# Optimization experiments

Hardware: AMD Instinct MI355X
Metric: run time of the kernel (lower is better)

## Reference

```python
import jax, jax.numpy as jnp
import numpy as np
import math

D_MODEL = 1024
N_HEADS = 16
D_K = D_MODEL // N_HEADS
B, S = 4, 2048


def setup_inputs() -> dict:
    key = jax.random.key(0)
    ks = jax.random.split(key, 11)
    std = 1.0 / math.sqrt(D_MODEL)
    inp = {
        "query": jax.random.normal(ks[0], (B, S, D_MODEL), dtype=jnp.float32),
        "key_in": jax.random.normal(ks[1], (B, S, D_MODEL), dtype=jnp.float32),
        "value": jax.random.normal(ks[2], (B, S, D_MODEL), dtype=jnp.float32),
        "Wq": jax.random.normal(ks[3], (D_MODEL, D_MODEL), dtype=jnp.float32) * std,
        "bq": jnp.zeros((D_MODEL,), dtype=jnp.float32),
        "Wk": jax.random.normal(ks[4], (D_MODEL, D_MODEL), dtype=jnp.float32) * std,
        "bk": jnp.zeros((D_MODEL,), dtype=jnp.float32),
        "Wv": jax.random.normal(ks[5], (D_MODEL, D_MODEL), dtype=jnp.float32) * std,
        "bv": jnp.zeros((D_MODEL,), dtype=jnp.float32),
        "Wo": jax.random.normal(ks[6], (D_MODEL, D_MODEL), dtype=jnp.float32) * std,
        "bo": jnp.zeros((D_MODEL,), dtype=jnp.float32),
    }
    return inp


def reference(query, key_in, value, Wq, bq, Wk, bk, Wv, bv, Wo, bo):
    b, s, _ = query.shape
    scale = math.sqrt(D_K)
    # projections: nn.Linear computes x @ W.T + b
    Q = (query @ Wq.T + bq).reshape(b, s, N_HEADS, D_K).transpose(0, 2, 1, 3)
    K = (key_in @ Wk.T + bk).reshape(b, s, N_HEADS, D_K).transpose(0, 2, 1, 3)
    V = (value @ Wv.T + bv).reshape(b, s, N_HEADS, D_K).transpose(0, 2, 1, 3)
    # [b, h, s, s]
    scores = jnp.einsum("bhqd,bhkd->bhqk", Q, K) / scale
    causal = jnp.tril(jnp.ones((s, s), dtype=bool))
    scores = jnp.where(causal[None, None, :, :], scores, jnp.float32(-1e9))
    attn = jax.nn.softmax(scores, axis=-1)
    out = jnp.einsum("bhqk,bhkd->bhqd", attn, V)
    out = out.transpose(0, 2, 1, 3).reshape(b, s, D_MODEL)
    return out @ Wo.T + bo
```

## Files before the change

kernel.cpp:

```cpp
#include <hip/hip_runtime.h>
#include <hip/hip_bf16.h>
#include <cstdint>

#define DM   1024
#define NH   16
#define DKK  64
#define BB   4
#define SS   2048

typedef __attribute__((ext_vector_type(8)))  short short8;
typedef __attribute__((ext_vector_type(4)))  float f32x4;
typedef __attribute__((ext_vector_type(16))) float f32x16;

__device__ __forceinline__ unsigned short f2bf(float f) {
    union { float f; uint32_t u; } v; v.f = f;
    uint32_t u = v.u;
    uint32_t r = (u + 0x7FFFu + ((u >> 16) & 1u)) >> 16;
    return (unsigned short)r;
}

#define GLL(src, dst) __builtin_amdgcn_global_load_lds(                      \
        (__attribute__((address_space(1))) void*)(src),                      \
        (__attribute__((address_space(3))) void*)(dst), 16, 0, 0)

__global__ void cvt_w(const float* __restrict__ wq, const float* __restrict__ wk,
                      const float* __restrict__ wv, const float* __restrict__ wo,
                      unsigned short* __restrict__ dst)
{
    int i = blockIdx.x * 256 + threadIdx.x;
    int a = i >> 17;
    int r = i & 131071;
    int j = r >> 7, kb = r & 127;
    int kbs = (kb & ~7) | ((kb ^ j) & 7);
    const float* s = (a == 0 ? wq : a == 1 ? wk : a == 2 ? wv : wo) + (size_t)j * 1024 + kbs * 8;
    float4 f0 = *(const float4*)(s);
    float4 f1 = *(const float4*)(s + 4);
    union { uint32_t u[4]; short8 s8; } c;
    asm("v_cvt_pk_bf16_f32 %0, %1, %2" : "=v"(c.u[0]) : "v"(f0.x), "v"(f0.y));
    asm("v_cvt_pk_bf16_f32 %0, %1, %2" : "=v"(c.u[1]) : "v"(f0.z), "v"(f0.w));
    asm("v_cvt_pk_bf16_f32 %0, %1, %2" : "=v"(c.u[2]) : "v"(f1.x), "v"(f1.y));
    asm("v_cvt_pk_bf16_f32 %0, %1, %2" : "=v"(c.u[3]) : "v"(f1.z), "v"(f1.w));
    *(short8*)(dst + ((size_t)a << 20) + (size_t)j * 1024 + kb * 8) = c.s8;
}

__global__ __launch_bounds__(256) void gemm_qkv(
        const float* __restrict__ Aq, const float* __restrict__ Ak, const float* __restrict__ Av,
        const unsigned short* __restrict__ Wq, const unsigned short* __restrict__ Wk,
        const unsigned short* __restrict__ Wv,
        const float* __restrict__ bq, const float* __restrict__ bk, const float* __restrict__ bv,
        unsigned short* __restrict__ Qo, unsigned short* __restrict__ Ko,
        unsigned short* __restrict__ Vo, const float qscale)
{
    const int orig = blockIdx.z * 512 + blockIdx.y * 8 + blockIdx.x;
    const int wid  = (orig & 7) * 192 + (orig >> 3);
    const int z    = wid >> 9;
    const int rem  = wid & 511;
    const int brow = (rem >> 3) * 128;
    const int bcol = (rem & 7) * 128;

    const float* A           = (z == 0) ? Aq : (z == 1) ? Ak : Av;
    const unsigned short* Bw = (z == 0) ? Wq : (z == 1) ? Wk : Wv;
    const float* bias        = (z == 0) ? bq : (z == 1) ? bk : bv;

    __shared__ __align__(16) unsigned short lA[128 * 64];
    __shared__ __align__(16) unsigned short lB[2][128 * 64];

    const int tid = threadIdx.x;
    const int w = tid >> 6, l = tid & 63;
    const int wr = (w >> 1) * 64, wc = (w & 1) * 64;
    const int lrow = l & 15;
    const int hi = l >> 4;
    const int sr = l >> 3, scb = l & 7;

    const float* aga[4];
    const unsigned short* bga[4];
    int awb[4], lbo[4];
#pragma unroll
    for (int i = 0; i < 4; ++i) {
        const int chunk = w * 4 + i;
        const int r = chunk * 8 + sr;
        aga[i] = A + (size_t)(brow + r) * 1024 + scb * 8;
        bga[i] = Bw + (size_t)(bcol + r) * 1024 + scb * 8;
        awb[i] = chunk * 1024 + sr * 128 + ((scb ^ sr) << 4);
        lbo[i] = chunk * 512;
    }

    f32x4 aX[4][2], aY[4][2];
    f32x4 acc[4][4] = {};

#pragma unroll
    for (int i = 0; i < 4; ++i) GLL(bga[i], lB[0] + lbo[i]);
#pragma unroll
    for (int i = 0; i < 4; ++i) { aX[i][0] = *(const f32x4*)(aga[i]); aX[i][1] = *(const f32x4*)(aga[i] + 4); }
#pragma unroll
    for (int i = 0; i < 4; ++i) { aY[i][0] = *(const f32x4*)(aga[i] + 64); aY[i][1] = *(const f32x4*)(aga[i] + 64 + 4); }

#define QKV_CVT(CUR)                                                                              \
    _Pragma("unroll")                                                                             \
    for (int i = 0; i < 4; ++i) {                                                                 \
        union { uint32_t u[4]; short8 s8; } c;                                                    \
        asm("v_cvt_pk_bf16_f32 %0, %1, %2" : "=v"(c.u[0]) : "v"(CUR[i][0][0]), "v"(CUR[i][0][1]));\
        asm("v_cvt_pk_bf16_f32 %0, %1, %2" : "=v"(c.u[1]) : "v"(CUR[i][0][2]), "v"(CUR[i][0][3]));\
        asm("v_cvt_pk_bf16_f32 %0, %1, %2" : "=v"(c.u[2]) : "v"(CUR[i][1][0]), "v"(CUR[i][1][1]));\
        asm("v_cvt_pk_bf16_f32 %0, %1, %2" : "=v"(c.u[3]) : "v"(CUR[i][1][2]), "v"(CUR[i][1][3]));\
        *(short8*)((char*)lA + awb[i]) = c.s8;                                                    \
    }

#define QKV_MFMA(LB)                                                                              \
    {                                                                                             \
        const unsigned short* lb = (LB);                                                          \
        __builtin_amdgcn_s_setprio(1);                                                            \
        _Pragma("unroll")                                                                         \
        for (int kk = 0; kk < 2; ++kk) {                                                          \
            short8 af[4], bf[4];                                                                  \
            _Pragma("unroll")                                                                     \
            for (int m = 0; m < 4; ++m) {                                                         \
                const int row = wr + m * 16 + lrow;                                               \
                const int pb = (kk * 4 + hi) ^ (row & 7);                                         \
                af[m] = *(const short8*)((const char*)lA + row * 128 + (pb << 4));                \
            }                                                                                     \
            _Pragma("unroll")                                                                     \
            for (int n = 0; n < 4; ++n) {                                                         \
                const int row = wc + n * 16 + lrow;                                               \
                const int pb = (kk * 4 + hi) ^ (row & 7);                                         \
                bf[n] = *(const short8*)((const char*)lb + row * 128 + (pb << 4));                \
            }                                                                                     \
            _Pragma("unroll")                                                                     \
            for (int m = 0; m < 4; ++m)                                                           \
                _Pragma("unroll")                                                                 \
                for (int n = 0; n < 4; ++n)                                                       \
                    acc[m][n] = __builtin_amdgcn_mfma_f32_16x16x32_bf16(af[m], bf[n], acc[m][n], 0, 0, 0); \
        }                                                                                         \
        __builtin_amdgcn_s_setprio(0);                                                            \
    }

    for (int t = 0; t < 14; t += 2) {
        QKV_CVT(aX);
        {
            const int ko = (t + 2) * 64;
#pragma unroll
            for (int i = 0; i < 4; ++i) { aX[i][0] = *(const f32x4*)(aga[i] + ko); aX[i][1] = *(const f32x4*)(aga[i] + ko + 4); }
            const int kb = (t + 1) * 64;
#pragma unroll
            for (int i = 0; i < 4; ++i) GLL(bga[i] + kb, lB[1] + lbo[i]);
        }
        asm volatile("s_waitcnt vmcnt(12) lgkmcnt(0)" ::: "memory");
        __builtin_amdgcn_s_barrier();
        QKV_MFMA(lB[0]);
        asm volatile("" ::: "memory");
        __builtin_amdgcn_s_barrier();
        QKV_CVT(aY);
        {
            const int ko = (t + 3) * 64;
#pragma unroll
            for (int i = 0; i < 4; ++i) { aY[i][0] = *(const f32x4*)(aga[i] + ko); aY[i][1] = *(const f32x4*)(aga[i] + ko + 4); }
            const int kb = (t + 2) * 64;
#pragma unroll
            for (int i = 0; i < 4; ++i) GLL(bga[i] + kb, lB[0] + lbo[i]);
        }
        asm volatile("s_waitcnt vmcnt(12) lgkmcnt(0)" ::: "memory");
        __builtin_amdgcn_s_barrier();
        QKV_MFMA(lB[1]);
        asm volatile("" ::: "memory");
        __builtin_amdgcn_s_barrier();
    }
    QKV_CVT(aX);
#pragma unroll
    for (int i = 0; i < 4; ++i) GLL(bga[i] + 15 * 64, lB[1] + lbo[i]);
    asm volatile("s_waitcnt vmcnt(4) lgkmcnt(0)" ::: "memory");
    __builtin_amdgcn_s_barrier();
    QKV_MFMA(lB[0]);
    asm volatile("" ::: "memory");
    __builtin_amdgcn_s_barrier();
    QKV_CVT(aY);
    asm volatile("s_waitcnt vmcnt(0) lgkmcnt(0)" ::: "memory");
    __builtin_amdgcn_s_barrier();
    QKV_MFMA(lB[1]);

    const float ascale = (z == 0) ? qscale : 1.0f;
#pragma unroll
    for (int m = 0; m < 4; ++m) {
#pragma unroll
        for (int n = 0; n < 4; ++n) {
            const int i0 = brow + wr + m * 16 + (l >> 4) * 4;
            const int j  = bcol + wc + n * 16 + lrow;
            const float bj = bias[j];
            const int hh = j >> 6, d = j & 63;
            if (z < 2) {
                unsigned short* Cb = (z == 0) ? Qo : Ko;
#pragma unroll
                for (int t = 0; t < 4; ++t) {
                    const int i = i0 + t;
                    const int b = i >> 11, s = i & 2047;
                    Cb[(((size_t)(b * NH + hh) * SS) + s) * DKK + d] = f2bf((acc[m][n][t] + bj) * ascale);
                }
            } else {
                const int b = i0 >> 11, s0 = i0 & 2047;
                ushort4 pk;
                pk.x = f2bf(acc[m][n][0] + bj);
                pk.y = f2bf(acc[m][n][1] + bj);
                pk.z = f2bf(acc[m][n][2] + bj);
                pk.w = f2bf(acc[m][n][3] + bj);
                *(ushort4*)(Vo + (((size_t)(b * NH + hh) * DKK) + d) * SS + s0) = pk;
            }
        }
    }
#undef QKV_CVT
#undef QKV_MFMA
}

__global__ __launch_bounds__(256) void gemm_out(
        const unsigned short* __restrict__ A,
        const unsigned short* __restrict__ Bw,
        const float* __restrict__ bias,
        float* __restrict__ Cout)
{
    const int orig = blockIdx.y * 8 + blockIdx.x;
    const int wid  = (orig & 7) * 64 + (orig >> 3);
    const int brow = (wid >> 3) * 128;
    const int bcol = (wid & 7) * 128;

    __shared__ __align__(16) unsigned short lA[128 * 64];
    __shared__ __align__(16) unsigned short lB[2][128 * 64];

    const int tid = threadIdx.x;
    const int w = tid >> 6, l = tid & 63;
    const int wr = (w >> 1) * 64, wc = (w & 1) * 64;
    const int lrow = l & 15;
    const int hi = l >> 4;
    const int sr = l >> 3, scb = l & 7;

    const unsigned short* aga[4];
    const unsigned short* bga[4];
    int awb[4], lbo[4];
#pragma unroll
    for (int i = 0; i < 4; ++i) {
        const int chunk = w * 4 + i;
        const int r = chunk * 8 + sr;
        aga[i] = A  + (size_t)(brow + r) * 1024 + scb * 8;
        bga[i] = Bw + (size_t)(bcol + r) * 1024 + scb * 8;
        awb[i] = chunk * 1024 + sr * 128 + ((scb ^ sr) << 4);
        lbo[i] = chunk * 512;
    }

    short8 aX[4], aY[4];
    f32x4 acc[4][4] = {};

#pragma unroll
    for (int i = 0; i < 4; ++i) GLL(bga[i], lB[0] + lbo[i]);
#pragma unroll
    for (int i = 0; i < 4; ++i) aX[i] = *(const short8*)(aga[i]);
#pragma unroll
    for (int i = 0; i < 4; ++i) aY[i] = *(const short8*)(aga[i] + 64);

#define OUT_WR(CUR)                                                     \
    _Pragma("unroll")                                                   \
    for (int i = 0; i < 4; ++i)                                         \
        *(short8*)((char*)lA + awb[i]) = CUR[i];

#define OUT_MFMA(LB)                                                                              \
    {                                                                                             \
        const unsigned short* lb = (LB);                                                          \
        __builtin_amdgcn_s_setprio(1);                                                            \
        _Pragma("unroll")                                                                         \
        for (int kk = 0; kk < 2; ++kk) {                                                          \
            short8 af[4], bf[4];                                                                  \
            _Pragma("unroll")                                                                     \
            for (int m = 0; m < 4; ++m) {                                                         \
                const int row = wr + m * 16 + lrow;                                               \
                const int pb = (kk * 4 + hi) ^ (row & 7);                                         \
                af[m] = *(const short8*)((const char*)lA + row * 128 + (pb << 4));                \
            }                                                                                     \
            _Pragma("unroll")                                                                     \
            for (int n = 0; n < 4; ++n) {                                                         \
                const int row = wc + n * 16 + lrow;                                               \
                const int pb = (kk * 4 + hi) ^ (row & 7);                                         \
                bf[n] = *(const short8*)((const char*)lb + row * 128 + (pb << 4));                \
            }                                                                                     \
            _Pragma("unroll")                                                                     \
            for (int m = 0; m < 4; ++m)                                                           \
                _Pragma("unroll")                                                                 \
                for (int n = 0; n < 4; ++n)                                                       \
                    acc[m][n] = __builtin_amdgcn_mfma_f32_16x16x32_bf16(af[m], bf[n], acc[m][n], 0, 0, 0); \
        }                                                                                         \
        __builtin_amdgcn_s_setprio(0);                                                            \
    }

    for (int t = 0; t < 14; t += 2) {
        OUT_WR(aX);
        {
            const int ko = (t + 2) * 64;
#pragma unroll
            for (int i = 0; i < 4; ++i) aX[i] = *(const short8*)(aga[i] + ko);
            const int kb = (t + 1) * 64;
#pragma unroll
            for (int i = 0; i < 4; ++i) GLL(bga[i] + kb, lB[1] + lbo[i]);
        }
        asm volatile("s_waitcnt vmcnt(8) lgkmcnt(0)" ::: "memory");
        __builtin_amdgcn_s_barrier();
        OUT_MFMA(lB[0]);
        asm volatile("" ::: "memory");
        __builtin_amdgcn_s_barrier();

        OUT_WR(aY);
        {
            const int ko = (t + 3) * 64;
#pragma unroll
            for (int i = 0; i < 4; ++i) aY[i] = *(const short8*)(aga[i] + ko);
            const int kb = (t + 2) * 64;
#pragma unroll
            for (int i = 0; i < 4; ++i) GLL(bga[i] + kb, lB[0] + lbo[i]);
        }
        asm volatile("s_waitcnt vmcnt(8) lgkmcnt(0)" ::: "memory");
        __builtin_amdgcn_s_barrier();
        OUT_MFMA(lB[1]);
        asm volatile("" ::: "memory");
        __builtin_amdgcn_s_barrier();
    }
    OUT_WR(aX);
#pragma unroll
    for (int i = 0; i < 4; ++i) GLL(bga[i] + 15 * 64, lB[1] + lbo[i]);
    asm volatile("s_waitcnt vmcnt(4) lgkmcnt(0)" ::: "memory");
    __builtin_amdgcn_s_barrier();
    OUT_MFMA(lB[0]);
    asm volatile("" ::: "memory");
    __builtin_amdgcn_s_barrier();
    OUT_WR(aY);
    asm volatile("s_waitcnt vmcnt(0) lgkmcnt(0)" ::: "memory");
    __builtin_amdgcn_s_barrier();
    OUT_MFMA(lB[1]);

#pragma unroll
    for (int m = 0; m < 4; ++m) {
#pragma unroll
        for (int n = 0; n < 4; ++n) {
            const int i0 = brow + wr + m * 16 + (l >> 4) * 4;
            const int j  = bcol + wc + n * 16 + lrow;
            const float bj = bias[j];
#pragma unroll
            for (int t = 0; t < 4; ++t)
                Cout[(size_t)(i0 + t) * DM + j] = acc[m][n][t] + bj;
        }
    }
#undef OUT_WR
#undef OUT_MFMA
}

__global__ __launch_bounds__(256) void attn_kernel(
        const unsigned short* __restrict__ Q,
        const unsigned short* __restrict__ K,
        const unsigned short* __restrict__ Vt,
        unsigned short* __restrict__ AO)
{
    const int flat = blockIdx.y * 16 + blockIdx.x;
    const int r8 = flat & 7, k8 = flat >> 3;
    const int bh = r8 * 8 + (k8 & 7);
    const int qchunk = 15 - (k8 >> 3);
    const int tid = threadIdx.x;
    const int w = tid >> 6, l = tid & 63;
    const int ln = l & 31, h = l >> 5;
    const int qb = qchunk * 128;
    const int q0w = qb + w * 32;

    __shared__ __align__(16) char lK[2][4096];
    __shared__ __align__(16) char lV[2][4096];

    const unsigned short* Qp = Q  + ((size_t)bh * SS + q0w) * DKK;
    const unsigned short* Kp = K  + (size_t)bh * SS * DKK;
    const unsigned short* Vp = Vt + (size_t)bh * DKK * SS;

    const int srow = tid >> 3, scb = tid & 7;
    const int swb = srow * 128 + ((scb * 16) ^ ((srow & 7) << 4));
    const unsigned short* ksrc = Kp + srow * DKK + scb * 8;
    const int vd = (scb < 4) ? srow : (srow + 32);
    const unsigned short* vsrc = Vp + (size_t)vd * SS + (scb & 3) * 8;

    int ka[4], va[4];
#pragma unroll
    for (int ks = 0; ks < 4; ++ks)
        ka[ks] = ln * 128 + ((ks * 32 + h * 16) ^ ((ln & 7) << 4));
#pragma unroll
    for (int c = 0; c < 4; ++c)
        va[c] = ln * 128 + ((c * 32 + h * 16) ^ ((ln & 7) << 4));

    short8 qf[4];
#pragma unroll
    for (int ks = 0; ks < 4; ++ks)
        qf[ks] = *(const short8*)(Qp + (size_t)ln * DKK + ks * 16 + h * 8);

    f32x16 o0 = {}, o1 = {};
    float lsum = 0.f;

    const int Tc = qb / 32;
    const int NT = Tc + 4;

    auto compute = [&](int t, int buf) {
        const char* kb = lK[buf];
        const char* vb = lV[buf];
        short8 kf[4];
#pragma unroll
        for (int ks = 0; ks < 4; ++ks) kf[ks] = *(const short8*)(kb + ka[ks]);

        f32x16 s = {};
        __builtin_amdgcn_s_setprio(1);
#pragma unroll
        for (int ks = 0; ks < 4; ++ks)
            s = __builtin_amdgcn_mfma_f32_32x32x16_bf16(kf[ks], qf[ks], s, 0, 0, 0);
        __builtin_amdgcn_s_setprio(0);

        const bool diag = (t == Tc + w);
#pragma unroll
        for (int r = 0; r < 16; ++r) {
            float e;
            asm("v_exp_f32 %0, %1" : "=v"(e) : "v"(s[r]));
            if (diag) {
                const int crow = (r & 3) + 8 * (r >> 2) + 4 * h;
                e = (crow > ln) ? 0.f : e;
            }
            s[r] = e;
            lsum += e;
        }

        uint32_t pk[8];
#pragma unroll
        for (int i = 0; i < 8; ++i) {
            uint32_t d;
            asm("v_cvt_pk_bf16_f32 %0, %1, %2" : "=v"(d) : "v"(s[2 * i]), "v"(s[2 * i + 1]));
            pk[i] = d;
        }
        asm("v_permlane32_swap_b32 %0, %1" : "+v"(pk[0]), "+v"(pk[2]));
        asm("v_permlane32_swap_b32 %0, %1" : "+v"(pk[1]), "+v"(pk[3]));
        asm("v_permlane32_swap_b32 %0, %1" : "+v"(pk[4]), "+v"(pk[6]));
        asm("v_permlane32_swap_b32 %0, %1" : "+v"(pk[5]), "+v"(pk[7]));

        union Ux { uint32_t u[4]; short8 s8; } pa0, pa1;
        pa0.u[0] = pk[0]; pa0.u[1] = pk[1]; pa0.u[2] = pk[2]; pa0.u[3] = pk[3];
        pa1.u[0] = pk[4]; pa1.u[1] = pk[5]; pa1.u[2] = pk[6]; pa1.u[3] = pk[7];

        short8 vf00 = *(const short8*)(vb + va[0]);
        short8 vf10 = *(const short8*)(vb + va[1]);
        short8 vf01 = *(const short8*)(vb + va[2]);
        short8 vf11 = *(const short8*)(vb + va[3]);

        __builtin_amdgcn_s_setprio(1);
        o0 = __builtin_amdgcn_mfma_f32_32x32x16_bf16(pa0.s8, vf00, o0, 0, 0, 0);
        o0 = __builtin_amdgcn_mfma_f32_32x32x16_bf16(pa1.s8, vf10, o0, 0, 0, 0);
        o1 = __builtin_amdgcn_mfma_f32_32x32x16_bf16(pa0.s8, vf01, o1, 0, 0, 0);
        o1 = __builtin_amdgcn_mfma_f32_32x32x16_bf16(pa1.s8, vf11, o1, 0, 0, 0);
        __builtin_amdgcn_s_setprio(0);
    };

    short8 kA = *(const short8*)(ksrc);
    short8 vA = *(const short8*)(vsrc);
    *(short8*)(&lK[0][swb]) = kA;
    *(short8*)(&lV[0][swb]) = vA;
    kA = *(const short8*)(ksrc + 2048);
    vA = *(const short8*)(vsrc + 32);
    short8 kB = {}, vB = {};
    __syncthreads();

    int t = 0, buf = 0;
    for (;;) {
        if (t + 2 < NT) {
            kB = *(const short8*)(ksrc + (size_t)(t + 2) * 2048);
            vB = *(const short8*)(vsrc + (size_t)(t + 2) * 32);
        }
        if (t <= Tc + w) compute(t, buf);
        if (t + 1 < NT) {
            *(short8*)(&lK[buf ^ 1][swb]) = kA;
            *(short8*)(&lV[buf ^ 1][swb]) = vA;
        }
        __syncthreads();
        buf ^= 1;
        if (++t == NT) break;

        if (t + 2 < NT) {
            kA = *(const short8*)(ksrc + (size_t)(t + 2) * 2048);
            vA = *(const short8*)(vsrc + (size_t)(t + 2) * 32);
        }
        if (t <= Tc + w) compute(t, buf);
        if (t + 1 < NT) {
            *(short8*)(&lK[buf ^ 1][swb]) = kB;
            *(short8*)(&lV[buf ^ 1][swb]) = vB;
        }
        __syncthreads();
        buf ^= 1;
        if (++t == NT) break;
    }

    lsum += __shfl_xor(lsum, 32, 64);
    const float rcp = 1.0f / lsum;

    const int bb = bh >> 4, hh = bh & 15;
#pragma unroll
    for (int r = 0; r < 16; ++r) {
        const int crow = (r & 3) + 8 * (r >> 2) + 4 * h;
        const float rl = __shfl(rcp, crow, 64);
        const size_t row = (size_t)(bb * SS + q0w + crow) * DM + hh * DKK;
        AO[row + ln]      = f2bf(o0[r] * rl);
        AO[row + 32 + ln] = f2bf(o1[r] * rl);
    }
}

extern "C" void kernel_launch(void* const* d_in, const int* in_sizes, int n_in,
                              void* d_out, int out_size, void* d_ws, size_t ws_size,
                              hipStream_t stream)
{
    const float* query  = (const float*)d_in[0];
    const float* key_in = (const float*)d_in[1];
    const float* value  = (const float*)d_in[2];
    const float* Wq = (const float*)d_in[3];
    const float* bq = (const float*)d_in[4];
    const float* Wk = (const float*)d_in[5];
    const float* bk = (const float*)d_in[6];
    const float* Wv = (const float*)d_in[7];
    const float* bv = (const float*)d_in[8];
    const float* Wo = (const float*)d_in[9];
    const float* bo = (const float*)d_in[10];

    const size_t NACT = (size_t)BB * SS * DM;
    const size_t NWT  = (size_t)DM * DM;

    unsigned short* ws  = (unsigned short*)d_ws;
    unsigned short* wqb = ws;
    unsigned short* wkb = wqb + NWT;
    unsigned short* wvb = wkb + NWT;
    unsigned short* wob = wvb + NWT;
    unsigned short* Qb  = wob + NWT;
    unsigned short* Kb  = Qb + NACT;
    unsigned short* Vtb = Kb + NACT;
    unsigned short* AOb = Vtb + NACT;

    cvt_w<<<2048, 256, 0, stream>>>(Wq, Wk, Wv, Wo, ws);

    const float QSCALE = 0.125f * 1.44269504088896f;
    dim3 gq(DM / 128, (BB * SS) / 128, 3);
    gemm_qkv<<<gq, 256, 0, stream>>>(query, key_in, value, wqb, wkb, wvb,
                                     bq, bk, bv, Qb, Kb, Vtb, QSCALE);

    attn_kernel<<<dim3(16, 64), 256, 0, stream>>>(Qb, Kb, Vtb, AOb);

    dim3 gg(DM / 128, (BB * SS) / 128);
    gemm_out<<<gg, 256, 0, stream>>>(AOb, wob, bo, (float*)d_out);
}
```

Measured before the change: 162.5 us.

## Pre-convert activations to bf16 and use 256x256 tiles in QKV GEMM

The fp32-to-bf16 conversion of query/key/value moves out of the QKV GEMM and into an extended conversion kernel that also handles the weights. The QKV GEMM then streams bf16 A and B tiles straight into LDS via global_load_lds and uses 256x256 tiles with 512 threads, double buffering and a phased MFMA schedule. This aims to cut register-side conversion work and increase operand reuse per block. The cost is an extra full read/write pass over all activations in the conversion kernel, and only 384 blocks, which may leave some compute units idle.

Measured after the change: 188.2 us. 15.9% more time.

```diff
diff --git a/kernel.cpp b/kernel.cpp
--- a/kernel.cpp
+++ b/kernel.cpp
@@ -23,16 +23,29 @@
         (__attribute__((address_space(1))) void*)(src),                      \
         (__attribute__((address_space(3))) void*)(dst), 16, 0, 0)
 
-__global__ void cvt_w(const float* __restrict__ wq, const float* __restrict__ wk,
-                      const float* __restrict__ wv, const float* __restrict__ wo,
-                      unsigned short* __restrict__ dst)
+__global__ void cvt_all(const float* __restrict__ q, const float* __restrict__ k,
+                        const float* __restrict__ v,
+                        const float* __restrict__ wq, const float* __restrict__ wk,
+                        const float* __restrict__ wv, const float* __restrict__ wo,
+                        unsigned short* __restrict__ dact, unsigned short* __restrict__ dw)
 {
     int i = blockIdx.x * 256 + threadIdx.x;
-    int a = i >> 17;
-    int r = i & 131071;
-    int j = r >> 7, kb = r & 127;
-    int kbs = (kb & ~7) | ((kb ^ j) & 7);
-    const float* s = (a == 0 ? wq : a == 1 ? wk : a == 2 ? wv : wo) + (size_t)j * 1024 + kbs * 8;
+    const float* s;
+    unsigned short* d;
+    if (i < 3145728) {
+        int a = i >> 20, r = i & 1048575;
+        int j = r >> 7, kb = r & 127;
+        int kbs = (kb & ~7) | ((kb ^ j) & 7);
+        s = (a == 0 ? q : a == 1 ? k : v) + (size_t)j * 1024 + kbs * 8;
+        d = dact + ((size_t)a << 23) + (size_t)j * 1024 + kb * 8;
+    } else {
+        int t = i - 3145728;
+        int a = t >> 17, r = t & 131071;
+        int j = r >> 7, kb = r & 127;
+        int kbs = (kb & ~7) | ((kb ^ j) & 7);
+        s = (a == 0 ? wq : a == 1 ? wk : a == 2 ? wv : wo) + (size_t)j * 1024 + kbs * 8;
+        d = dw + ((size_t)a << 20) + (size_t)j * 1024 + kb * 8;
+    }
     float4 f0 = *(const float4*)(s);
     float4 f1 = *(const float4*)(s + 4);
     union { uint32_t u[4]; short8 s8; } c;
@@ -40,150 +53,118 @@
     asm("v_cvt_pk_bf16_f32 %0, %1, %2" : "=v"(c.u[1]) : "v"(f0.z), "v"(f0.w));
     asm("v_cvt_pk_bf16_f32 %0, %1, %2" : "=v"(c.u[2]) : "v"(f1.x), "v"(f1.y));
     asm("v_cvt_pk_bf16_f32 %0, %1, %2" : "=v"(c.u[3]) : "v"(f1.z), "v"(f1.w));
-    *(short8*)(dst + ((size_t)a << 20) + (size_t)j * 1024 + kb * 8) = c.s8;
+    *(short8*)d = c.s8;
 }
 
-__global__ __launch_bounds__(256) void gemm_qkv(
-        const float* __restrict__ Aq, const float* __restrict__ Ak, const float* __restrict__ Av,
+__global__ __launch_bounds__(512, 2) void gemm_qkv(
+        const unsigned short* __restrict__ Act,
         const unsigned short* __restrict__ Wq, const unsigned short* __restrict__ Wk,
         const unsigned short* __restrict__ Wv,
         const float* __restrict__ bq, const float* __restrict__ bk, const float* __restrict__ bv,
         unsigned short* __restrict__ Qo, unsigned short* __restrict__ Ko,
         unsigned short* __restrict__ Vo, const float qscale)
 {
-    const int orig = blockIdx.z * 512 + blockIdx.y * 8 + blockIdx.x;
-    const int wid  = (orig & 7) * 192 + (orig >> 3);
-    const int z    = wid >> 9;
-    const int rem  = wid & 511;
-    const int brow = (rem >> 3) * 128;
-    const int bcol = (rem & 7) * 128;
-
-    const float* A           = (z == 0) ? Aq : (z == 1) ? Ak : Av;
+    const int orig = blockIdx.x;
+    const int wid  = (orig & 7) * 48 + (orig >> 3);
+    const int z    = wid >> 7;
+    const int r    = wid & 127;
+    const int brow = (r >> 2) * 256;
+    const int bcol = (r & 3) * 256;
+
+    const unsigned short* A  = Act + ((size_t)z << 23);
     const unsigned short* Bw = (z == 0) ? Wq : (z == 1) ? Wk : Wv;
     const float* bias        = (z == 0) ? bq : (z == 1) ? bk : bv;
 
-    __shared__ __align__(16) unsigned short lA[128 * 64];
-    __shared__ __align__(16) unsigned short lB[2][128 * 64];
+    __shared__ __align__(16) unsigned short lA[2][2][8192];
+    __shared__ __align__(16) unsigned short lB[2][2][8192];
 
     const int tid = threadIdx.x;
     const int w = tid >> 6, l = tid & 63;
-    const int wr = (w >> 1) * 64, wc = (w & 1) * 64;
-    const int lrow = l & 15;
-    const int hi = l >> 4;
-    const int sr = l >> 3, scb = l & 7;
-
-    const float* aga[4];
-    const unsigned short* bga[4];
-    int awb[4], lbo[4];
-#pragma unroll
-    for (int i = 0; i < 4; ++i) {
-        const int chunk = w * 4 + i;
-        const int r = chunk * 8 + sr;
-        aga[i] = A + (size_t)(brow + r) * 1024 + scb * 8;
-        bga[i] = Bw + (size_t)(bcol + r) * 1024 + scb * 8;
-        awb[i] = chunk * 1024 + sr * 128 + ((scb ^ sr) << 4);
-        lbo[i] = chunk * 512;
-    }
-
-    f32x4 aX[4][2], aY[4][2];
-    f32x4 acc[4][4] = {};
-
-#pragma unroll
-    for (int i = 0; i < 4; ++i) GLL(bga[i], lB[0] + lbo[i]);
-#pragma unroll
-    for (int i = 0; i < 4; ++i) { aX[i][0] = *(const f32x4*)(aga[i]); aX[i][1] = *(const f32x4*)(aga[i] + 4); }
-#pragma unroll
-    for (int i = 0; i < 4; ++i) { aY[i][0] = *(const f32x4*)(aga[i] + 64); aY[i][1] = *(const f32x4*)(aga[i] + 64 + 4); }
-
-#define QKV_CVT(CUR)                                                                              \
-    _Pragma("unroll")                                                                             \
-    for (int i = 0; i < 4; ++i) {                                                                 \
-        union { uint32_t u[4]; short8 s8; } c;                                                    \
-        asm("v_cvt_pk_bf16_f32 %0, %1, %2" : "=v"(c.u[0]) : "v"(CUR[i][0][0]), "v"(CUR[i][0][1]));\
-        asm("v_cvt_pk_bf16_f32 %0, %1, %2" : "=v"(c.u[1]) : "v"(CUR[i][0][2]), "v"(CUR[i][0][3]));\
-        asm("v_cvt_pk_bf16_f32 %0, %1, %2" : "=v"(c.u[2]) : "v"(CUR[i][1][0]), "v"(CUR[i][1][1]));\
-        asm("v_cvt_pk_bf16_f32 %0, %1, %2" : "=v"(c.u[3]) : "v"(CUR[i][1][2]), "v"(CUR[i][1][3]));\
-        *(short8*)((char*)lA + awb[i]) = c.s8;                                                    \
-    }
-
-#define QKV_MFMA(LB)                                                                              \
-    {                                                                                             \
-        const unsigned short* lb = (LB);                                                          \
-        __builtin_amdgcn_s_setprio(1);                                                            \
-        _Pragma("unroll")                                                                         \
-        for (int kk = 0; kk < 2; ++kk) {                                                          \
-            short8 af[4], bf[4];                                                                  \
-            _Pragma("unroll")                                                                     \
-            for (int m = 0; m < 4; ++m) {                                                         \
-                const int row = wr + m * 16 + lrow;                                               \
-                const int pb = (kk * 4 + hi) ^ (row & 7);                                         \
-                af[m] = *(const short8*)((const char*)lA + row * 128 + (pb << 4));                \
-            }                                                                                     \
-            _Pragma("unroll")                                                                     \
-            for (int n = 0; n < 4; ++n) {                                                         \
-                const int row = wc + n * 16 + lrow;                                               \
-                const int pb = (kk * 4 + hi) ^ (row & 7);                                         \
-                bf[n] = *(const short8*)((const char*)lb + row * 128 + (pb << 4));                \
-            }                                                                                     \
-            _Pragma("unroll")                                                                     \
-            for (int m = 0; m < 4; ++m)                                                           \
-                _Pragma("unroll")                                                                 \
-                for (int n = 0; n < 4; ++n)                                                       \
-                    acc[m][n] = __builtin_amdgcn_mfma_f32_16x16x32_bf16(af[m], bf[n], acc[m][n], 0, 0, 0); \
-        }                                                                                         \
-        __builtin_amdgcn_s_setprio(0);                                                            \
-    }
-
-    for (int t = 0; t < 14; t += 2) {
-        QKV_CVT(aX);
-        {
-            const int ko = (t + 2) * 64;
-#pragma unroll
-            for (int i = 0; i < 4; ++i) { aX[i][0] = *(const f32x4*)(aga[i] + ko); aX[i][1] = *(const f32x4*)(aga[i] + ko + 4); }
-            const int kb = (t + 1) * 64;
-#pragma unroll
-            for (int i = 0; i < 4; ++i) GLL(bga[i] + kb, lB[1] + lbo[i]);
-        }
-        asm volatile("s_waitcnt vmcnt(12) lgkmcnt(0)" ::: "memory");
-        __builtin_amdgcn_s_barrier();
-        QKV_MFMA(lB[0]);
-        asm volatile("" ::: "memory");
-        __builtin_amdgcn_s_barrier();
-        QKV_CVT(aY);
-        {
-            const int ko = (t + 3) * 64;
-#pragma unroll
-            for (int i = 0; i < 4; ++i) { aY[i][0] = *(const f32x4*)(aga[i] + ko); aY[i][1] = *(const f32x4*)(aga[i] + ko + 4); }
-            const int kb = (t + 2) * 64;
-#pragma unroll
-            for (int i = 0; i < 4; ++i) GLL(bga[i] + kb, lB[0] + lbo[i]);
-        }
-        asm volatile("s_waitcnt vmcnt(12) lgkmcnt(0)" ::: "memory");
-        __builtin_amdgcn_s_barrier();
-        QKV_MFMA(lB[1]);
-        asm volatile("" ::: "memory");
-        __builtin_amdgcn_s_barrier();
-    }
-    QKV_CVT(aX);
-#pragma unroll
-    for (int i = 0; i < 4; ++i) GLL(bga[i] + 15 * 64, lB[1] + lbo[i]);
-    asm volatile("s_waitcnt vmcnt(4) lgkmcnt(0)" ::: "memory");
+    const int wm = w >> 2, wn = w & 3;
+    const int lrow = l & 15, hi = l >> 4;
+
+    const unsigned short* Asrc = A  + (size_t)(brow + (tid >> 3)) * 1024 + (tid & 7) * 8;
+    const unsigned short* Bsrc = Bw + (size_t)(bcol + (tid >> 3)) * 1024 + (tid & 7) * 8;
+
+    int axr[2];
+    axr[0] = ((hi ^ (lrow & 7)) << 4);
+    axr[1] = (((4 + hi) ^ (lrow & 7)) << 4);
+
+    short8 bfr[4][2];
+    f32x4 acc[8][4] = {};
+
+#define STG_A(KT, H)                                                                         \
+    { GLL(Asrc + (size_t)((H) * 128) * 1024 + (KT) * 64,      &lA[(KT) & 1][H][w * 512]);    \
+      GLL(Asrc + (size_t)((H) * 128 + 64) * 1024 + (KT) * 64, &lA[(KT) & 1][H][4096 + w * 512]); }
+#define STG_B(KT, H)                                                                         \
+    { GLL(Bsrc + (size_t)((H) * 128) * 1024 + (KT) * 64,      &lB[(KT) & 1][H][w * 512]);    \
+      GLL(Bsrc + (size_t)((H) * 128 + 64) * 1024 + (KT) * 64, &lB[(KT) & 1][H][4096 + w * 512]); }
+#define VM4 asm volatile("s_waitcnt vmcnt(4)" ::: "memory")
+#define VM0 asm volatile("s_waitcnt vmcnt(0)" ::: "memory")
+
+#define PH(KT, MQ, READB, STG, WAIT)                                                         \
+    {                                                                                        \
+        const char* la_ = (const char*)lA[(KT) & 1][wm];                                     \
+        const char* lb_ = (const char*)lB[(KT) & 1][wn >> 1];                                \
+        if (READB) {                                                                         \
+            _Pragma("unroll") for (int n = 0; n < 4; ++n)                                    \
+            _Pragma("unroll") for (int kk = 0; kk < 2; ++kk)                                 \
+                bfr[n][kk] = *(const short8*)(lb_ + ((wn & 1) * 64 + n * 16 + lrow) * 128 + axr[kk]); \
+        }                                                                                    \
+        short8 af_[2][2];                                                                    \
+        _Pragma("unroll") for (int j = 0; j < 2; ++j)                                        \
+        _Pragma("unroll") for (int kk = 0; kk < 2; ++kk)                                     \
+            af_[j][kk] = *(const short8*)(la_ + (((MQ) * 2 + j) * 16 + lrow) * 128 + axr[kk]); \
+        STG;                                                                                 \
+        WAIT;                                                                                \
+        __builtin_amdgcn_s_barrier();                                                        \
+        asm volatile("s_waitcnt lgkmcnt(0)" ::: "memory");                                   \
+        __builtin_amdgcn_sched_barrier(0);                                                   \
+        __builtin_amdgcn_s_setprio(1);                                                       \
+        _Pragma("unroll") for (int j = 0; j < 2; ++j)                                        \
+        _Pragma("unroll") for (int n = 0; n < 4; ++n)                                        \
+        _Pragma("unroll") for (int kk = 0; kk < 2; ++kk)                                     \
+            acc[(MQ) * 2 + j][n] = __builtin_amdgcn_mfma_f32_16x16x32_bf16(                  \
+                af_[j][kk], bfr[n][kk], acc[(MQ) * 2 + j][n], 0, 0, 0);                      \
+        __builtin_amdgcn_s_setprio(0);                                                       \
+        __builtin_amdgcn_s_barrier();                                                        \
+    }
+
+    STG_A(0, 0); STG_A(0, 1); STG_B(0, 0); STG_B(0, 1); STG_B(1, 0); STG_B(1, 1);
+    VM4;
     __builtin_amdgcn_s_barrier();
-    QKV_MFMA(lB[0]);
-    asm volatile("" ::: "memory");
-    __builtin_amdgcn_s_barrier();
-    QKV_CVT(aY);
-    asm volatile("s_waitcnt vmcnt(0) lgkmcnt(0)" ::: "memory");
-    __builtin_amdgcn_s_barrier();
-    QKV_MFMA(lB[1]);
+
+    for (int i = 0; i < 7; ++i) {
+        const int kt = 2 * i;
+        PH(kt,     0, 1, STG_A(kt + 1, 0), (void)0);
+        PH(kt,     1, 0, STG_A(kt + 1, 1), (void)0);
+        PH(kt,     2, 0, STG_B(kt + 2, 0), (void)0);
+        PH(kt,     3, 0, STG_B(kt + 2, 1), VM4);
+        PH(kt + 1, 0, 1, STG_A(kt + 2, 0), (void)0);
+        PH(kt + 1, 1, 0, STG_A(kt + 2, 1), (void)0);
+        PH(kt + 1, 2, 0, STG_B(kt + 3, 0), (void)0);
+        PH(kt + 1, 3, 0, STG_B(kt + 3, 1), VM4);
+    }
+    PH(14, 0, 1, STG_A(15, 0), (void)0);
+    PH(14, 1, 0, STG_A(15, 1), (void)0);
+    PH(14, 2, 0, (void)0, (void)0);
+    PH(14, 3, 0, (void)0, VM0);
+    PH(15, 0, 1, (void)0, (void)0);
+    PH(15, 1, 0, (void)0, (void)0);
+    PH(15, 2, 0, (void)0, (void)0);
+    PH(15, 3, 0, (void)0, (void)0);
+
+#undef PH
+#undef STG_A
+#undef STG_B
 
     const float ascale = (z == 0) ? qscale : 1.0f;
 #pragma unroll
-    for (int m = 0; m < 4; ++m) {
+    for (int m = 0; m < 8; ++m) {
 #pragma unroll
         for (int n = 0; n < 4; ++n) {
-            const int i0 = brow + wr + m * 16 + (l >> 4) * 4;
-            const int j  = bcol + wc + n * 16 + lrow;
+            const int i0 = brow + wm * 128 + m * 16 + hi * 4;
+            const int j  = bcol + wn * 64 + n * 16 + lrow;
             const float bj = bias[j];
             const int hh = j >> 6, d = j & 63;
             if (z < 2) {
@@ -205,8 +186,6 @@
             }
         }
     }
-#undef QKV_CVT
-#undef QKV_MFMA
 }
 
 __global__ __launch_bounds__(256) void gemm_out(
@@ -521,22 +500,22 @@
     const size_t NACT = (size_t)BB * SS * DM;
     const size_t NWT  = (size_t)DM * DM;
 
-    unsigned short* ws  = (unsigned short*)d_ws;
-    unsigned short* wqb = ws;
-    unsigned short* wkb = wqb + NWT;
-    unsigned short* wvb = wkb + NWT;
-    unsigned short* wob = wvb + NWT;
-    unsigned short* Qb  = wob + NWT;
-    unsigned short* Kb  = Qb + NACT;
-    unsigned short* Vtb = Kb + NACT;
-    unsigned short* AOb = Vtb + NACT;
-
-    cvt_w<<<2048, 256, 0, stream>>>(Wq, Wk, Wv, Wo, ws);
+    unsigned short* ws   = (unsigned short*)d_ws;
+    unsigned short* actb = ws;
+    unsigned short* wqb  = actb + 3 * NACT;
+    unsigned short* wkb  = wqb + NWT;
+    unsigned short* wvb  = wkb + NWT;
+    unsigned short* wob  = wvb + NWT;
+    unsigned short* Qb   = wob + NWT;
+    unsigned short* Kb   = Qb + NACT;
+    unsigned short* Vtb  = Kb + NACT;
+    unsigned short* AOb  = Vtb + NACT;
+
+    cvt_all<<<14336, 256, 0, stream>>>(query, key_in, value, Wq, Wk, Wv, Wo, actb, wqb);
 
     const float QSCALE = 0.125f * 1.44269504088896f;
-    dim3 gq(DM / 128, (BB * SS) / 128, 3);
-    gemm_qkv<<<gq, 256, 0, stream>>>(query, key_in, value, wqb, wkb, wvb,
-                                     bq, bk, bv, Qb, Kb, Vtb, QSCALE);
+    gemm_qkv<<<384, 512, 0, stream>>>(actb, wqb, wkb, wvb,
+                                      bq, bk, bv, Qb, Kb, Vtb, QSCALE);
 
     attn_kernel<<<dim3(16, 64), 256, 0, stream>>>(Qb, Kb, Vtb, AOb);
 
```

## Pre-convert fp32 activations to bf16 in a fused conversion kernel before QKV GEMM

Applied to the files above, without the earlier changes.

Extends the weight conversion kernel to also convert query, key and value activations to bf16 in a workspace, using a grid-stride loop. The QKV GEMM then loads bf16 A tiles directly and writes them to LDS without in-loop conversion, halving A-load bytes per tile and lowering register use. The cost is an extra full read and write pass over the activations before the GEMM.

New measurement: 175.9 us. 1.08x slower.

```diff
diff --git a/kernel.cpp b/kernel.cpp
--- a/kernel.cpp
+++ b/kernel.cpp
@@ -23,28 +23,41 @@
         (__attribute__((address_space(1))) void*)(src),                      \
         (__attribute__((address_space(3))) void*)(dst), 16, 0, 0)
 
-__global__ void cvt_w(const float* __restrict__ wq, const float* __restrict__ wk,
-                      const float* __restrict__ wv, const float* __restrict__ wo,
-                      unsigned short* __restrict__ dst)
+__global__ void cvt_all(const float* __restrict__ q, const float* __restrict__ k,
+                        const float* __restrict__ v,
+                        const float* __restrict__ wq, const float* __restrict__ wk,
+                        const float* __restrict__ wv, const float* __restrict__ wo,
+                        unsigned short* __restrict__ dact, unsigned short* __restrict__ dw)
 {
-    int i = blockIdx.x * 256 + threadIdx.x;
-    int a = i >> 17;
-    int r = i & 131071;
-    int j = r >> 7, kb = r & 127;
-    int kbs = (kb & ~7) | ((kb ^ j) & 7);
-    const float* s = (a == 0 ? wq : a == 1 ? wk : a == 2 ? wv : wo) + (size_t)j * 1024 + kbs * 8;
-    float4 f0 = *(const float4*)(s);
-    float4 f1 = *(const float4*)(s + 4);
-    union { uint32_t u[4]; short8 s8; } c;
-    asm("v_cvt_pk_bf16_f32 %0, %1, %2" : "=v"(c.u[0]) : "v"(f0.x), "v"(f0.y));
-    asm("v_cvt_pk_bf16_f32 %0, %1, %2" : "=v"(c.u[1]) : "v"(f0.z), "v"(f0.w));
-    asm("v_cvt_pk_bf16_f32 %0, %1, %2" : "=v"(c.u[2]) : "v"(f1.x), "v"(f1.y));
-    asm("v_cvt_pk_bf16_f32 %0, %1, %2" : "=v"(c.u[3]) : "v"(f1.z), "v"(f1.w));
-    *(short8*)(dst + ((size_t)a << 20) + (size_t)j * 1024 + kb * 8) = c.s8;
+    const int NTOT = 3670016;
+    for (int i = blockIdx.x * 256 + threadIdx.x; i < NTOT; i += 2048 * 256) {
+        const float* s;
+        unsigned short* d;
+        if (i < 3145728) {
+            int a = i >> 20, off = i & 1048575;
+            s = (a == 0 ? q : a == 1 ? k : v) + (size_t)off * 8;
+            d = dact + ((size_t)a << 23) + (size_t)off * 8;
+        } else {
+            int t = i - 3145728;
+            int a = t >> 17, r = t & 131071;
+            int j = r >> 7, kb = r & 127;
+            int kbs = (kb & ~7) | ((kb ^ j) & 7);
+            s = (a == 0 ? wq : a == 1 ? wk : a == 2 ? wv : wo) + (size_t)j * 1024 + kbs * 8;
+            d = dw + ((size_t)a << 20) + (size_t)j * 1024 + kb * 8;
+        }
+        float4 f0 = *(const float4*)(s);
+        float4 f1 = *(const float4*)(s + 4);
+        union { uint32_t u[4]; short8 s8; } c;
+        asm("v_cvt_pk_bf16_f32 %0, %1, %2" : "=v"(c.u[0]) : "v"(f0.x), "v"(f0.y));
+        asm("v_cvt_pk_bf16_f32 %0, %1, %2" : "=v"(c.u[1]) : "v"(f0.z), "v"(f0.w));
+        asm("v_cvt_pk_bf16_f32 %0, %1, %2" : "=v"(c.u[2]) : "v"(f1.x), "v"(f1.y));
+        asm("v_cvt_pk_bf16_f32 %0, %1, %2" : "=v"(c.u[3]) : "v"(f1.z), "v"(f1.w));
+        *(short8*)d = c.s8;
+    }
 }
 
 __global__ __launch_bounds__(256) void gemm_qkv(
-        const float* __restrict__ Aq, const float* __restrict__ Ak, const float* __restrict__ Av,
+        const unsigned short* __restrict__ Act,
         const unsigned short* __restrict__ Wq, const unsigned short* __restrict__ Wk,
         const unsigned short* __restrict__ Wv,
         const float* __restrict__ bq, const float* __restrict__ bk, const float* __restrict__ bv,
@@ -58,7 +71,7 @@
     const int brow = (rem >> 3) * 128;
     const int bcol = (rem & 7) * 128;
 
-    const float* A           = (z == 0) ? Aq : (z == 1) ? Ak : Av;
+    const unsigned short* A  = Act + ((size_t)z << 23);
     const unsigned short* Bw = (z == 0) ? Wq : (z == 1) ? Wk : Wv;
     const float* bias        = (z == 0) ? bq : (z == 1) ? bk : bv;
 
@@ -72,39 +85,33 @@
     const int hi = l >> 4;
     const int sr = l >> 3, scb = l & 7;
 
-    const float* aga[4];
+    const unsigned short* aga[4];
     const unsigned short* bga[4];
     int awb[4], lbo[4];
 #pragma unroll
     for (int i = 0; i < 4; ++i) {
         const int chunk = w * 4 + i;
         const int r = chunk * 8 + sr;
-        aga[i] = A + (size_t)(brow + r) * 1024 + scb * 8;
+        aga[i] = A  + (size_t)(brow + r) * 1024 + scb * 8;
         bga[i] = Bw + (size_t)(bcol + r) * 1024 + scb * 8;
         awb[i] = chunk * 1024 + sr * 128 + ((scb ^ sr) << 4);
         lbo[i] = chunk * 512;
     }
 
-    f32x4 aX[4][2], aY[4][2];
+    short8 aX[4], aY[4];
     f32x4 acc[4][4] = {};
 
 #pragma unroll
     for (int i = 0; i < 4; ++i) GLL(bga[i], lB[0] + lbo[i]);
 #pragma unroll
-    for (int i = 0; i < 4; ++i) { aX[i][0] = *(const f32x4*)(aga[i]); aX[i][1] = *(const f32x4*)(aga[i] + 4); }
-#pragma unroll
-    for (int i = 0; i < 4; ++i) { aY[i][0] = *(const f32x4*)(aga[i] + 64); aY[i][1] = *(const f32x4*)(aga[i] + 64 + 4); }
-
-#define QKV_CVT(CUR)                                                                              \
-    _Pragma("unroll")                                                                             \
-    for (int i = 0; i < 4; ++i) {                                                                 \
-        union { uint32_t u[4]; short8 s8; } c;                                                    \
-        asm("v_cvt_pk_bf16_f32 %0, %1, %2" : "=v"(c.u[0]) : "v"(CUR[i][0][0]), "v"(CUR[i][0][1]));\
-        asm("v_cvt_pk_bf16_f32 %0, %1, %2" : "=v"(c.u[1]) : "v"(CUR[i][0][2]), "v"(CUR[i][0][3]));\
-        asm("v_cvt_pk_bf16_f32 %0, %1, %2" : "=v"(c.u[2]) : "v"(CUR[i][1][0]), "v"(CUR[i][1][1]));\
-        asm("v_cvt_pk_bf16_f32 %0, %1, %2" : "=v"(c.u[3]) : "v"(CUR[i][1][2]), "v"(CUR[i][1][3]));\
-        *(short8*)((char*)lA + awb[i]) = c.s8;                                                    \
-    }
+    for (int i = 0; i < 4; ++i) aX[i] = *(const short8*)(aga[i]);
+#pragma unroll
+    for (int i = 0; i < 4; ++i) aY[i] = *(const short8*)(aga[i] + 64);
+
+#define QKV_WR(CUR)                                                     \
+    _Pragma("unroll")                                                   \
+    for (int i = 0; i < 4; ++i)                                         \
+        *(short8*)((char*)lA + awb[i]) = CUR[i];
 
 #define QKV_MFMA(LB)                                                                              \
     {                                                                                             \
@@ -135,36 +142,37 @@
     }
 
     for (int t = 0; t < 14; t += 2) {
-        QKV_CVT(aX);
+        QKV_WR(aX);
         {
             const int ko = (t + 2) * 64;
 #pragma unroll
-            for (int i = 0; i < 4; ++i) { aX[i][0] = *(const f32x4*)(aga[i] + ko); aX[i][1] = *(const f32x4*)(aga[i] + ko + 4); }
+            for (int i = 0; i < 4; ++i) aX[i] = *(const short8*)(aga[i] + ko);
             const int kb = (t + 1) * 64;
 #pragma unroll
             for (int i = 0; i < 4; ++i) GLL(bga[i] + kb, lB[1] + lbo[i]);
         }
-        asm volatile("s_waitcnt vmcnt(12) lgkmcnt(0)" ::: "memory");
+        asm volatile("s_waitcnt vmcnt(8) lgkmcnt(0)" ::: "memory");
         __builtin_amdgcn_s_barrier();
         QKV_MFMA(lB[0]);
         asm volatile("" ::: "memory");
         __builtin_amdgcn_s_barrier();
-        QKV_CVT(aY);
+
+        QKV_WR(aY);
         {
             const int ko = (t + 3) * 64;
 #pragma unroll
-            for (int i = 0; i < 4; ++i) { aY[i][0] = *(const f32x4*)(aga[i] + ko); aY[i][1] = *(const f32x4*)(aga[i] + ko + 4); }
+            for (int i = 0; i < 4; ++i) aY[i] = *(const short8*)(aga[i] + ko);
             const int kb = (t + 2) * 64;
 #pragma unroll
             for (int i = 0; i < 4; ++i) GLL(bga[i] + kb, lB[0] + lbo[i]);
         }
-        asm volatile("s_waitcnt vmcnt(12) lgkmcnt(0)" ::: "memory");
+        asm volatile("s_waitcnt vmcnt(8) lgkmcnt(0)" ::: "memory");
         __builtin_amdgcn_s_barrier();
         QKV_MFMA(lB[1]);
         asm volatile("" ::: "memory");
         __builtin_amdgcn_s_barrier();
     }
-    QKV_CVT(aX);
+    QKV_WR(aX);
 #pragma unroll
     for (int i = 0; i < 4; ++i) GLL(bga[i] + 15 * 64, lB[1] + lbo[i]);
     asm volatile("s_waitcnt vmcnt(4) lgkmcnt(0)" ::: "memory");
@@ -172,17 +180,20 @@
     QKV_MFMA(lB[0]);
     asm volatile("" ::: "memory");
     __builtin_amdgcn_s_barrier();
-    QKV_CVT(aY);
+    QKV_WR(aY);
     asm volatile("s_waitcnt vmcnt(0) lgkmcnt(0)" ::: "memory");
     __builtin_amdgcn_s_barrier();
     QKV_MFMA(lB[1]);
 
+#undef QKV_WR
+#undef QKV_MFMA
+
     const float ascale = (z == 0) ? qscale : 1.0f;
 #pragma unroll
     for (int m = 0; m < 4; ++m) {
 #pragma unroll
         for (int n = 0; n < 4; ++n) {
-            const int i0 = brow + wr + m * 16 + (l >> 4) * 4;
+            const int i0 = brow + wr + m * 16 + hi * 4;
             const int j  = bcol + wc + n * 16 + lrow;
             const float bj = bias[j];
             const int hh = j >> 6, d = j & 63;
@@ -205,8 +216,6 @@
             }
         }
     }
-#undef QKV_CVT
-#undef QKV_MFMA
 }
 
 __global__ __launch_bounds__(256) void gemm_out(
@@ -521,21 +530,22 @@
     const size_t NACT = (size_t)BB * SS * DM;
     const size_t NWT  = (size_t)DM * DM;
 
-    unsigned short* ws  = (unsigned short*)d_ws;
-    unsigned short* wqb = ws;
-    unsigned short* wkb = wqb + NWT;
-    unsigned short* wvb = wkb + NWT;
-    unsigned short* wob = wvb + NWT;
-    unsigned short* Qb  = wob + NWT;
-    unsigned short* Kb  = Qb + NACT;
-    unsigned short* Vtb = Kb + NACT;
-    unsigned short* AOb = Vtb + NACT;
-
-    cvt_w<<<2048, 256, 0, stream>>>(Wq, Wk, Wv, Wo, ws);
+    unsigned short* ws   = (unsigned short*)d_ws;
+    unsigned short* actb = ws;
+    unsigned short* wqb  = actb + 3 * NACT;
+    unsigned short* wkb  = wqb + NWT;
+    unsigned short* wvb  = wkb + NWT;
+    unsigned short* wob  = wvb + NWT;
+    unsigned short* Qb   = wob + NWT;
+    unsigned short* Kb   = Qb + NACT;
+    unsigned short* Vtb  = Kb + NACT;
+    unsigned short* AOb  = Vtb + NACT;
+
+    cvt_all<<<2048, 256, 0, stream>>>(query, key_in, value, Wq, Wk, Wv, Wo, actb, wqb);
 
     const float QSCALE = 0.125f * 1.44269504088896f;
-    dim3 gq(DM / 128, (BB * SS) / 128, 3);
-    gemm_qkv<<<gq, 256, 0, stream>>>(query, key_in, value, wqb, wkb, wvb,
+    dim3 gq(8, 64, 3);
+    gemm_qkv<<<gq, 256, 0, stream>>>(actb, wqb, wkb, wvb,
                                      bq, bk, bv, Qb, Kb, Vtb, QSCALE);
 
     attn_kernel<<<dim3(16, 64), 256, 0, stream>>>(Qb, Kb, Vtb, AOb);
```
